# Kernel tuning notes

Measured on AMD Instinct MI355X. Metric: run time of the kernel, lower is better.

## Reference

```python
import jax, jax.numpy as jnp
import numpy as np
import math

N_NODES = 50000
N_EDGES = 1600000
HIDDEN = 128
HEADS = 4
HEAD_DIM = HIDDEN // HEADS


def setup_inputs() -> dict:
    key = jax.random.key(0)
    ks = jax.random.split(key, 10)
    s_in = 1.0 / math.sqrt(4)
    s_out = 1.0 / math.sqrt(HIDDEN)
    return {
        "x": jax.random.normal(ks[0], (N_NODES, 4), dtype=jnp.float32),
        "edge_index": jax.random.randint(ks[1], (2, N_EDGES), 0, N_NODES, dtype=jnp.int32),
        "Wq": jax.random.uniform(ks[2], (HIDDEN, 4), jnp.float32, -s_in, s_in),
        "bq": jax.random.uniform(ks[3], (HIDDEN,), jnp.float32, -s_in, s_in),
        "Wk": jax.random.uniform(ks[4], (HIDDEN, 4), jnp.float32, -s_in, s_in),
        "bk": jax.random.uniform(ks[5], (HIDDEN,), jnp.float32, -s_in, s_in),
        "Wv": jax.random.uniform(ks[6], (HIDDEN, 4), jnp.float32, -s_in, s_in),
        "bv": jax.random.uniform(ks[7], (HIDDEN,), jnp.float32, -s_in, s_in),
        "Wo": jax.random.uniform(ks[8], (4, HIDDEN), jnp.float32, -s_out, s_out),
        "bo": jax.random.uniform(ks[9], (4,), jnp.float32, -s_out, s_out),
    }


def reference(x, edge_index, Wq, bq, Wk, bk, Wv, bv, Wo, bo):
    n = x.shape[0]
    # projections 4 -> hidden, split into heads: [N, H, D]
    Q = (x @ Wq.T + bq).reshape(n, HEADS, HEAD_DIM)
    K = (x @ Wk.T + bk).reshape(n, HEADS, HEAD_DIM)
    V = (x @ Wv.T + bv).reshape(n, HEADS, HEAD_DIM)
    row, col = edge_index[0], edge_index[1]
    # per-edge, per-head scores: [E, H]
    scores = jnp.einsum('ehd,ehd->eh', Q[row], K[col]) / math.sqrt(HEAD_DIM)
    # NB: original applies softmax over ALL edges (dim=0), per head
    w = jax.nn.softmax(scores, axis=0)  # [E, H]
    # attended[col] += w * V[row]  -> segment-sum over destination nodes
    contrib = w[:, :, None] * V[row]  # [E, H, D]
    attended = jax.ops.segment_sum(contrib, col, num_segments=n)  # [N, H, D]
    attended = attended.reshape(n, HIDDEN)
    out = attended @ Wo.T + bo  # dropout is identity in eval
    return out + x
```

## Files before the change

kernel.cpp:

```cpp
#include <hip/hip_runtime.h>
#include <math.h>

#define NNODES 50000
#define NEDGES 1600000
#define BINSZ 128
#define NBINS 391
#define NBLK 1000
#define EPB (NEDGES / NBLK)
#define BCAP 4608
#define SCALE 0.17677669529663687f

__device__ __forceinline__ void compute_C_entry(int t,
        const float* Wq, const float* bq, const float* Wk, const float* bk,
        const float* Wv, const float* bv, const float* Wo, float* C_lds) {
    if (t < 64) {
        int h = t >> 4, a = (t >> 2) & 3, b = t & 3;
        float s = 0.f;
        for (int k = 0; k < 32; k++) s += Wq[(h * 32 + k) * 4 + a] * Wk[(h * 32 + k) * 4 + b];
        C_lds[t] = s;
    } else if (t < 80) {
        int h = (t - 64) >> 2, b = (t - 64) & 3;
        float s = 0.f;
        for (int k = 0; k < 32; k++) s += bq[h * 32 + k] * Wk[(h * 32 + k) * 4 + b];
        C_lds[t] = s;
    } else if (t < 96) {
        int h = (t - 80) >> 2, a = (t - 80) & 3;
        float s = 0.f;
        for (int k = 0; k < 32; k++) s += Wq[(h * 32 + k) * 4 + a] * bk[h * 32 + k];
        C_lds[t] = s;
    } else if (t < 100) {
        int h = t - 96;
        float s = 0.f;
        for (int k = 0; k < 32; k++) s += bq[h * 32 + k] * bk[h * 32 + k];
        C_lds[t] = s;
    } else if (t < 164) {
        int i = t - 100;
        int h = i >> 4, o = (i >> 2) & 3, a = i & 3;
        float s = 0.f;
        for (int k = 0; k < 32; k++) s += Wo[o * 128 + h * 32 + k] * Wv[(h * 32 + k) * 4 + a];
        C_lds[t] = s;
    } else if (t < 180) {
        int i = t - 164;
        int h = i >> 2, o = i & 3;
        float s = 0.f;
        for (int k = 0; k < 32; k++) s += Wo[o * 128 + h * 32 + k] * bv[h * 32 + k];
        C_lds[t] = s;
    }
}

__global__ __launch_bounds__(256) void k_binA(const int* __restrict__ ei,
                                              unsigned* __restrict__ chunks,
                                              unsigned* __restrict__ dir) {
    __shared__ unsigned raw[EPB];
    __shared__ unsigned srt[EPB];
    __shared__ int h0[512];
    __shared__ int h1[512];
    int t = threadIdx.x, blk = blockIdx.x;
    for (int i = t; i < 512; i += 256) h0[i] = 0;
    __syncthreads();
    int e0 = blk * EPB;
    for (int i = t; i < EPB; i += 256) {
        int r = ei[e0 + i];
        int c = ei[NEDGES + e0 + i];
        raw[i] = ((unsigned)c << 16) | (unsigned)r;
        atomicAdd(&h0[c >> 7], 1);
    }
    __syncthreads();
    int* src = h0; int* dst = h1;
    for (int off = 1; off < 512; off <<= 1) {
        for (int i = t; i < 512; i += 256)
            dst[i] = src[i] + (i >= off ? src[i - off] : 0);
        __syncthreads();
        int* tmp = src; src = dst; dst = tmp;
    }
    for (int i = t; i < 512; i += 256) dst[i] = i ? src[i - 1] : 0;
    __syncthreads();
    for (int i = t; i < EPB; i += 256) {
        unsigned v = raw[i];
        int b = v >> 23;
        int pos = atomicAdd(&dst[b], 1);
        srt[pos] = v;
    }
    __syncthreads();
    uint4* co = (uint4*)(chunks + (size_t)blk * EPB);
    const uint4* si = (const uint4*)srt;
    for (int i = t; i < EPB / 4; i += 256) co[i] = si[i];
    for (int b = t; b < NBINS; b += 256) {
        int start = b ? src[b - 1] : 0;
        int len = src[b] - start;
        dir[(size_t)blk * NBINS + b] = ((unsigned)start << 16) | (unsigned)len;
    }
}

__global__ __launch_bounds__(256) void k_accum(
        const unsigned* __restrict__ chunks, const unsigned* __restrict__ dir,
        const float* __restrict__ x,
        const float* __restrict__ Wq, const float* __restrict__ bq,
        const float* __restrict__ Wk, const float* __restrict__ bk,
        const float* __restrict__ Wv, const float* __restrict__ bv,
        const float* __restrict__ Wo,
        float* __restrict__ acc, float* __restrict__ pS) {
    __shared__ float Cl[192];
    __shared__ float pe[BINSZ][20];
    __shared__ unsigned raw[BCAP];
    __shared__ unsigned short srt[BCAP];
    __shared__ int hist[BINSZ];
    __shared__ int ofs[BINSZ];
    __shared__ int nv;
    __shared__ float sw[4][4];
    int bin = blockIdx.x;
    int t = threadIdx.x;
    int base = bin << 7;
    compute_C_entry(t, Wq, bq, Wk, bk, Wv, bv, Wo, Cl);
    if (t < BINSZ) hist[t] = 0;
    if (t == 0) nv = 0;
    __syncthreads();
    if (t < BINSZ) {
        int node = base + t;
        if (node < NNODES) {
            float4 xv = ((const float4*)x)[node];
            float pr[20];
#pragma unroll
            for (int h = 0; h < 4; h++) {
#pragma unroll
                for (int a = 0; a < 4; a++) {
                    float g = Cl[80 + h * 4 + a]
                            + Cl[h * 16 + a * 4 + 0] * xv.x + Cl[h * 16 + a * 4 + 1] * xv.y
                            + Cl[h * 16 + a * 4 + 2] * xv.z + Cl[h * 16 + a * 4 + 3] * xv.w;
                    pr[h * 4 + a] = g * SCALE;
                }
                float e = Cl[96 + h]
                        + Cl[64 + h * 4 + 0] * xv.x + Cl[64 + h * 4 + 1] * xv.y
                        + Cl[64 + h * 4 + 2] * xv.z + Cl[64 + h * 4 + 3] * xv.w;
                pr[16 + h] = e * SCALE;
            }
#pragma unroll
            for (int q = 0; q < 5; q++) ((float4*)pe[t])[q] = ((const float4*)pr)[q];
        }
    }
    for (int blk = t; blk < NBLK; blk += 256) {
        unsigned d = dir[(size_t)blk * NBINS + bin];
        int start = d >> 16;
        int len = d & 0xFFFFu;
        const unsigned* cp = chunks + (size_t)blk * EPB + start;
        for (int j = 0; j < len; j++) {
            unsigned v = cp[j];
            int pos = atomicAdd(&nv, 1);
            if (pos < BCAP) {
                raw[pos] = v;
                atomicAdd(&hist[(int)(v >> 16) - base], 1);
            }
        }
    }
    __syncthreads();
    if (t < 64) {
        int a0 = hist[2 * t], a1 = hist[2 * t + 1];
        int pair = a0 + a1;
        int p = pair;
#pragma unroll
        for (int off = 1; off < 64; off <<= 1) {
            int u = __shfl_up(p, off, 64);
            if (t >= off) p += u;
        }
        int excl = p - pair;
        hist[2 * t] = excl; hist[2 * t + 1] = excl + a0;
        ofs[2 * t] = excl;  ofs[2 * t + 1] = excl + a0;
    }
    __syncthreads();
    int nval = nv < BCAP ? nv : BCAP;
    for (int i = t; i < nval; i += 256) {
        unsigned v = raw[i];
        int lc = (int)(v >> 16) - base;
        int pos = atomicAdd(&ofs[lc], 1);
        srt[pos] = (unsigned short)(v & 0xFFFFu);
    }
    __syncthreads();
    int nl = t >> 1;
    int sub = t & 1;
    int node = base + nl;
    int sBeg = hist[nl], sEnd = ofs[nl];
    float4 g0 = ((const float4*)pe[nl])[0];
    float4 g1 = ((const float4*)pe[nl])[1];
    float4 g2 = ((const float4*)pe[nl])[2];
    float4 g3 = ((const float4*)pe[nl])[3];
    float4 eh = ((const float4*)pe[nl])[4];
    float S0 = 0.f, S1 = 0.f, S2 = 0.f, S3 = 0.f;
    float4 y0 = {0, 0, 0, 0}, y1 = y0, y2 = y0, y3 = y0;
    for (int i = sBeg + sub; i < sEnd; i += 2) {
        int r = (int)srt[i];
        float4 xv = ((const float4*)x)[r];
        float p0 = __expf(xv.x * g0.x + xv.y * g0.y + xv.z * g0.z + xv.w * g0.w + eh.x);
        float p1 = __expf(xv.x * g1.x + xv.y * g1.y + xv.z * g1.z + xv.w * g1.w + eh.y);
        float p2 = __expf(xv.x * g2.x + xv.y * g2.y + xv.z * g2.z + xv.w * g2.w + eh.z);
        float p3 = __expf(xv.x * g3.x + xv.y * g3.y + xv.z * g3.z + xv.w * g3.w + eh.w);
        y0.x += p0 * xv.x; y0.y += p0 * xv.y; y0.z += p0 * xv.z; y0.w += p0 * xv.w;
        y1.x += p1 * xv.x; y1.y += p1 * xv.y; y1.z += p1 * xv.z; y1.w += p1 * xv.w;
        y2.x += p2 * xv.x; y2.y += p2 * xv.y; y2.z += p2 * xv.z; y2.w += p2 * xv.w;
        y3.x += p3 * xv.x; y3.y += p3 * xv.y; y3.z += p3 * xv.z; y3.w += p3 * xv.w;
        S0 += p0; S1 += p1; S2 += p2; S3 += p3;
    }
    y0.x += __shfl_xor(y0.x, 1); y0.y += __shfl_xor(y0.y, 1);
    y0.z += __shfl_xor(y0.z, 1); y0.w += __shfl_xor(y0.w, 1);
    y1.x += __shfl_xor(y1.x, 1); y1.y += __shfl_xor(y1.y, 1);
    y1.z += __shfl_xor(y1.z, 1); y1.w += __shfl_xor(y1.w, 1);
    y2.x += __shfl_xor(y2.x, 1); y2.y += __shfl_xor(y2.y, 1);
    y2.z += __shfl_xor(y2.z, 1); y2.w += __shfl_xor(y2.w, 1);
    y3.x += __shfl_xor(y3.x, 1); y3.y += __shfl_xor(y3.y, 1);
    y3.z += __shfl_xor(y3.z, 1); y3.w += __shfl_xor(y3.w, 1);
    S0 += __shfl_xor(S0, 1); S1 += __shfl_xor(S1, 1);
    S2 += __shfl_xor(S2, 1); S3 += __shfl_xor(S3, 1);
    if (node < NNODES) {
        float4* ap = (float4*)(acc + (size_t)node * 20);
        float4 sv = {S0, S1, S2, S3};
        if (sub == 0) { ap[0] = y0; ap[2] = y2; ap[4] = sv; }
        else { ap[1] = y1; ap[3] = y3; }
    }
    float z0 = (sub == 0 && node < NNODES) ? S0 : 0.f;
    float z1 = (sub == 0 && node < NNODES) ? S1 : 0.f;
    float z2 = (sub == 0 && node < NNODES) ? S2 : 0.f;
    float z3 = (sub == 0 && node < NNODES) ? S3 : 0.f;
#pragma unroll
    for (int off = 1; off < 64; off <<= 1) {
        z0 += __shfl_xor(z0, off); z1 += __shfl_xor(z1, off);
        z2 += __shfl_xor(z2, off); z3 += __shfl_xor(z3, off);
    }
    int w = t >> 6;
    if ((t & 63) == 0) { sw[w][0] = z0; sw[w][1] = z1; sw[w][2] = z2; sw[w][3] = z3; }
    __syncthreads();
    if (t == 0) {
        float4 v;
        v.x = sw[0][0] + sw[1][0] + sw[2][0] + sw[3][0];
        v.y = sw[0][1] + sw[1][1] + sw[2][1] + sw[3][1];
        v.z = sw[0][2] + sw[1][2] + sw[2][2] + sw[3][2];
        v.w = sw[0][3] + sw[1][3] + sw[2][3] + sw[3][3];
        ((float4*)pS)[bin] = v;
    }
}

__global__ __launch_bounds__(256) void k_out(
        const float* __restrict__ acc, const float* __restrict__ pS,
        const float* __restrict__ Wq, const float* __restrict__ bq,
        const float* __restrict__ Wk, const float* __restrict__ bk,
        const float* __restrict__ Wv, const float* __restrict__ bv,
        const float* __restrict__ Wo, const float* __restrict__ bo,
        const float* __restrict__ x, float* __restrict__ out) {
    __shared__ float Cl[192];
    __shared__ float sd[4][4];
    __shared__ float dd[4];
    int t = threadIdx.x;
    compute_C_entry(t, Wq, bq, Wk, bk, Wv, bv, Wo, Cl);
    float s0 = 0.f, s1 = 0.f, s2 = 0.f, s3 = 0.f;
    for (int i = t; i < NBINS; i += 256) {
        float4 v = ((const float4*)pS)[i];
        s0 += v.x; s1 += v.y; s2 += v.z; s3 += v.w;
    }
#pragma unroll
    for (int off = 1; off < 64; off <<= 1) {
        s0 += __shfl_xor(s0, off); s1 += __shfl_xor(s1, off);
        s2 += __shfl_xor(s2, off); s3 += __shfl_xor(s3, off);
    }
    int w = t >> 6;
    if ((t & 63) == 0) { sd[w][0] = s0; sd[w][1] = s1; sd[w][2] = s2; sd[w][3] = s3; }
    __syncthreads();
    if (t < 4) dd[t] = 1.f / (sd[0][t] + sd[1][t] + sd[2][t] + sd[3][t]);
    __syncthreads();
    int i = blockIdx.x * blockDim.x + t;
    if (i >= NNODES) return;
    const float4* ap = (const float4*)(acc + (size_t)i * 20);
    float4 y[4] = {ap[0], ap[1], ap[2], ap[3]};
    float4 S = ap[4];
    float Sv[4] = {S.x, S.y, S.z, S.w};
    float di[4] = {dd[0], dd[1], dd[2], dd[3]};
    float o[4];
#pragma unroll
    for (int oo = 0; oo < 4; oo++) {
        float a = bo[oo];
#pragma unroll
        for (int h = 0; h < 4; h++) {
            float m = Cl[100 + h * 16 + oo * 4 + 0] * y[h].x
                    + Cl[100 + h * 16 + oo * 4 + 1] * y[h].y
                    + Cl[100 + h * 16 + oo * 4 + 2] * y[h].z
                    + Cl[100 + h * 16 + oo * 4 + 3] * y[h].w
                    + Cl[164 + h * 4 + oo] * Sv[h];
            a += di[h] * m;
        }
        o[oo] = a;
    }
    float4 xv = ((const float4*)x)[i];
    float4 ov;
    ov.x = o[0] + xv.x; ov.y = o[1] + xv.y; ov.z = o[2] + xv.z; ov.w = o[3] + xv.w;
    ((float4*)out)[i] = ov;
}

extern "C" void kernel_launch(void* const* d_in, const int* in_sizes, int n_in,
                              void* d_out, int out_size, void* d_ws, size_t ws_size,
                              hipStream_t stream) {
    const float* x = (const float*)d_in[0];
    const int* ei = (const int*)d_in[1];
    const float* Wq = (const float*)d_in[2];
    const float* bq = (const float*)d_in[3];
    const float* Wk = (const float*)d_in[4];
    const float* bk = (const float*)d_in[5];
    const float* Wv = (const float*)d_in[6];
    const float* bv = (const float*)d_in[7];
    const float* Wo = (const float*)d_in[8];
    const float* bo = (const float*)d_in[9];
    float* out = (float*)d_out;

    float* fws = (float*)d_ws;
    float* acc = fws;
    float* pS = acc + (size_t)NNODES * 20;
    unsigned* chunks = (unsigned*)(pS + (size_t)NBINS * 4 + 4);
    unsigned* dir = chunks + (size_t)NEDGES;

    k_binA<<<NBLK, 256, 0, stream>>>(ei, chunks, dir);
    k_accum<<<NBINS, 256, 0, stream>>>(chunks, dir, x, Wq, bq, Wk, bk, Wv, bv, Wo, acc, pS);
    k_out<<<(NNODES + 255) / 256, 256, 0, stream>>>(acc, pS,
                                                    Wq, bq, Wk, bk, Wv, bv, Wo, bo, x, out);
}
```

Before: 55.32 us.

## Split per-bin accumulation across two blocks and replace atomic gather with prefix scan

```diff
diff --git a/kernel.cpp b/kernel.cpp
--- a/kernel.cpp
+++ b/kernel.cpp
@@ -7,7 +7,8 @@
 #define NBINS 391
 #define NBLK 1000
 #define EPB (NEDGES / NBLK)
-#define BCAP 4608
+#define HALF 500
+#define PCAP 2560
 #define SCALE 0.17677669529663687f
 
 __device__ __forceinline__ void compute_C_entry(int t,
@@ -53,32 +54,41 @@
                                               unsigned* __restrict__ dir) {
     __shared__ unsigned raw[EPB];
     __shared__ unsigned srt[EPB];
-    __shared__ int h0[512];
-    __shared__ int h1[512];
+    __shared__ int hist[512];
+    __shared__ int ofs[512];
     int t = threadIdx.x, blk = blockIdx.x;
-    for (int i = t; i < 512; i += 256) h0[i] = 0;
+    hist[t] = 0; hist[t + 256] = 0;
     __syncthreads();
     int e0 = blk * EPB;
     for (int i = t; i < EPB; i += 256) {
         int r = ei[e0 + i];
         int c = ei[NEDGES + e0 + i];
         raw[i] = ((unsigned)c << 16) | (unsigned)r;
-        atomicAdd(&h0[c >> 7], 1);
-    }
-    __syncthreads();
-    int* src = h0; int* dst = h1;
-    for (int off = 1; off < 512; off <<= 1) {
-        for (int i = t; i < 512; i += 256)
-            dst[i] = src[i] + (i >= off ? src[i - off] : 0);
-        __syncthreads();
-        int* tmp = src; src = dst; dst = tmp;
-    }
-    for (int i = t; i < 512; i += 256) dst[i] = i ? src[i - 1] : 0;
+        atomicAdd(&hist[c >> 7], 1);
+    }
+    __syncthreads();
+    if (t < 64) {
+        int v[8], run = 0;
+#pragma unroll
+        for (int j = 0; j < 8; j++) { v[j] = hist[8 * t + j]; run += v[j]; }
+        int p = run;
+#pragma unroll
+        for (int off = 1; off < 64; off <<= 1) {
+            int u = __shfl_up(p, off, 64);
+            if (t >= off) p += u;
+        }
+        int base = p - run;
+#pragma unroll
+        for (int j = 0; j < 8; j++) {
+            hist[8 * t + j] = base;
+            ofs[8 * t + j] = base;
+            base += v[j];
+        }
+    }
     __syncthreads();
     for (int i = t; i < EPB; i += 256) {
         unsigned v = raw[i];
-        int b = v >> 23;
-        int pos = atomicAdd(&dst[b], 1);
+        int pos = atomicAdd(&ofs[v >> 23], 1);
         srt[pos] = v;
     }
     __syncthreads();
@@ -86,8 +96,8 @@
     const uint4* si = (const uint4*)srt;
     for (int i = t; i < EPB / 4; i += 256) co[i] = si[i];
     for (int b = t; b < NBINS; b += 256) {
-        int start = b ? src[b - 1] : 0;
-        int len = src[b] - start;
+        int start = hist[b];
+        int len = ofs[b] - start;
         dir[(size_t)blk * NBINS + b] = ((unsigned)start << 16) | (unsigned)len;
     }
 }
@@ -102,18 +112,19 @@
         float* __restrict__ acc, float* __restrict__ pS) {
     __shared__ float Cl[192];
     __shared__ float pe[BINSZ][20];
-    __shared__ unsigned raw[BCAP];
-    __shared__ unsigned short srt[BCAP];
+    __shared__ unsigned raw[PCAP];
+    __shared__ unsigned short srt[PCAP];
     __shared__ int hist[BINSZ];
     __shared__ int ofs[BINSZ];
-    __shared__ int nv;
+    __shared__ int wsum[4];
     __shared__ float sw[4][4];
-    int bin = blockIdx.x;
+    int bid = blockIdx.x;
+    int bin = bid >> 1;
+    int part = bid & 1;
     int t = threadIdx.x;
     int base = bin << 7;
     compute_C_entry(t, Wq, bq, Wk, bk, Wv, bv, Wo, Cl);
     if (t < BINSZ) hist[t] = 0;
-    if (t == 0) nv = 0;
     __syncthreads();
     if (t < BINSZ) {
         int node = base + t;
@@ -138,36 +149,62 @@
             for (int q = 0; q < 5; q++) ((float4*)pe[t])[q] = ((const float4*)pr)[q];
         }
     }
-    for (int blk = t; blk < NBLK; blk += 256) {
-        unsigned d = dir[(size_t)blk * NBINS + bin];
-        int start = d >> 16;
-        int len = d & 0xFFFFu;
-        const unsigned* cp = chunks + (size_t)blk * EPB + start;
+    int blk0 = part * HALF + t;
+    int blk1 = part * HALF + t + 256;
+    unsigned d0 = 0, d1 = 0;
+    int cnt = 0;
+    if (t < HALF) { d0 = dir[(size_t)blk0 * NBINS + bin]; cnt += d0 & 0xFFFFu; }
+    if (t + 256 < HALF) { d1 = dir[(size_t)blk1 * NBINS + bin]; cnt += d1 & 0xFFFFu; }
+    int lane = t & 63, w = t >> 6;
+    int p = cnt;
+#pragma unroll
+    for (int off = 1; off < 64; off <<= 1) {
+        int u = __shfl_up(p, off, 64);
+        if (lane >= off) p += u;
+    }
+    if (lane == 63) wsum[w] = p;
+    __syncthreads();
+    int wbase = 0;
+#pragma unroll
+    for (int ww = 0; ww < 4; ww++) wbase += (ww < w) ? wsum[ww] : 0;
+    int off0 = wbase + p - cnt;
+    int nval = wsum[0] + wsum[1] + wsum[2] + wsum[3];
+    if (nval > PCAP) nval = PCAP;
+    if (t < HALF) {
+        int len = d0 & 0xFFFFu;
+        const unsigned* cp = chunks + (size_t)blk0 * EPB + (d0 >> 16);
         for (int j = 0; j < len; j++) {
             unsigned v = cp[j];
-            int pos = atomicAdd(&nv, 1);
-            if (pos < BCAP) {
-                raw[pos] = v;
-                atomicAdd(&hist[(int)(v >> 16) - base], 1);
-            }
+            if (off0 < PCAP) raw[off0] = v;
+            atomicAdd(&hist[(int)(v >> 16) - base], 1);
+            off0++;
+        }
+    }
+    if (t + 256 < HALF) {
+        int len = d1 & 0xFFFFu;
+        const unsigned* cp = chunks + (size_t)blk1 * EPB + (d1 >> 16);
+        for (int j = 0; j < len; j++) {
+            unsigned v = cp[j];
+            if (off0 < PCAP) raw[off0] = v;
+            atomicAdd(&hist[(int)(v >> 16) - base], 1);
+            off0++;
         }
     }
     __syncthreads();
     if (t < 64) {
         int a0 = hist[2 * t], a1 = hist[2 * t + 1];
         int pair = a0 + a1;
-        int p = pair;
+        int pp = pair;
 #pragma unroll
         for (int off = 1; off < 64; off <<= 1) {
-            int u = __shfl_up(p, off, 64);
-            if (t >= off) p += u;
-        }
-        int excl = p - pair;
+            int u = __shfl_up(pp, off, 64);
+            if (t >= off) pp += u;
+        }
+        int excl = pp - pair;
         hist[2 * t] = excl; hist[2 * t + 1] = excl + a0;
         ofs[2 * t] = excl;  ofs[2 * t + 1] = excl + a0;
     }
     __syncthreads();
-    int nval = nv < BCAP ? nv : BCAP;
     for (int i = t; i < nval; i += 256) {
         unsigned v = raw[i];
         int lc = (int)(v >> 16) - base;
@@ -210,7 +247,7 @@
     S0 += __shfl_xor(S0, 1); S1 += __shfl_xor(S1, 1);
     S2 += __shfl_xor(S2, 1); S3 += __shfl_xor(S3, 1);
     if (node < NNODES) {
-        float4* ap = (float4*)(acc + (size_t)node * 20);
+        float4* ap = (float4*)(acc + ((size_t)part * NNODES + node) * 20);
         float4 sv = {S0, S1, S2, S3};
         if (sub == 0) { ap[0] = y0; ap[2] = y2; ap[4] = sv; }
         else { ap[1] = y1; ap[3] = y3; }
@@ -224,7 +261,6 @@
         z0 += __shfl_xor(z0, off); z1 += __shfl_xor(z1, off);
         z2 += __shfl_xor(z2, off); z3 += __shfl_xor(z3, off);
     }
-    int w = t >> 6;
     if ((t & 63) == 0) { sw[w][0] = z0; sw[w][1] = z1; sw[w][2] = z2; sw[w][3] = z3; }
     __syncthreads();
     if (t == 0) {
@@ -233,7 +269,7 @@
         v.y = sw[0][1] + sw[1][1] + sw[2][1] + sw[3][1];
         v.z = sw[0][2] + sw[1][2] + sw[2][2] + sw[3][2];
         v.w = sw[0][3] + sw[1][3] + sw[2][3] + sw[3][3];
-        ((float4*)pS)[bin] = v;
+        ((float4*)pS)[bid] = v;
     }
 }
 
@@ -250,7 +286,7 @@
     int t = threadIdx.x;
     compute_C_entry(t, Wq, bq, Wk, bk, Wv, bv, Wo, Cl);
     float s0 = 0.f, s1 = 0.f, s2 = 0.f, s3 = 0.f;
-    for (int i = t; i < NBINS; i += 256) {
+    for (int i = t; i < 2 * NBINS; i += 256) {
         float4 v = ((const float4*)pS)[i];
         s0 += v.x; s1 += v.y; s2 += v.z; s3 += v.w;
     }
@@ -266,9 +302,18 @@
     __syncthreads();
     int i = blockIdx.x * blockDim.x + t;
     if (i >= NNODES) return;
-    const float4* ap = (const float4*)(acc + (size_t)i * 20);
-    float4 y[4] = {ap[0], ap[1], ap[2], ap[3]};
-    float4 S = ap[4];
+    const float4* a0 = (const float4*)(acc + (size_t)i * 20);
+    const float4* a1 = (const float4*)(acc + ((size_t)NNODES + i) * 20);
+    float4 y[4], S;
+#pragma unroll
+    for (int q = 0; q < 4; q++) {
+        float4 u = a0[q], v = a1[q];
+        y[q].x = u.x + v.x; y[q].y = u.y + v.y; y[q].z = u.z + v.z; y[q].w = u.w + v.w;
+    }
+    {
+        float4 u = a0[4], v = a1[4];
+        S.x = u.x + v.x; S.y = u.y + v.y; S.z = u.z + v.z; S.w = u.w + v.w;
+    }
     float Sv[4] = {S.x, S.y, S.z, S.w};
     float di[4] = {dd[0], dd[1], dd[2], dd[3]};
     float o[4];
@@ -309,12 +354,12 @@
 
     float* fws = (float*)d_ws;
     float* acc = fws;
-    float* pS = acc + (size_t)NNODES * 20;
-    unsigned* chunks = (unsigned*)(pS + (size_t)NBINS * 4 + 4);
+    float* pS = acc + (size_t)2 * NNODES * 20;
+    unsigned* chunks = (unsigned*)(pS + (size_t)2 * NBINS * 4 + 4);
     unsigned* dir = chunks + (size_t)NEDGES;
 
     k_binA<<<NBLK, 256, 0, stream>>>(ei, chunks, dir);
-    k_accum<<<NBINS, 256, 0, stream>>>(chunks, dir, x, Wq, bq, Wk, bk, Wv, bv, Wo, acc, pS);
+    k_accum<<<2 * NBINS, 256, 0, stream>>>(chunks, dir, x, Wq, bq, Wk, bk, Wv, bv, Wo, acc, pS);
     k_out<<<(NNODES + 255) / 256, 256, 0, stream>>>(acc, pS,
                                                     Wq, bq, Wk, bk, Wv, bv, Wo, bo, x, out);
 }
```

Result: faster. 51.42 us (-7.0%).
